# Kernel optimization log

Measured on AMD Instinct MI355X. Metric: run time of the kernel, lower is better.

The kernel has to match this reference:

```python
import jax, jax.numpy as jnp
import numpy as np

B, NQ, D, NH, DH = 16, 300, 256, 8, 32
L, P, FFN = 3, 4, 1024
LEVEL_SHAPES = [(80, 80), (40, 40), (20, 20)]
S = sum(h * w for h, w in LEVEL_SHAPES)  # 8400
EPS = 1e-5

PARAM_NAMES = ['wq', 'bq', 'wk', 'bk', 'wv', 'bv', 'wo', 'bo', 'ln1_g', 'ln1_b',
               'w_off', 'b_off', 'w_aw', 'b_aw', 'w_val', 'b_val', 'w_out', 'b_out',
               'ln2_g', 'ln2_b', 'w_fc1', 'b_fc1', 'w_fc2', 'b_fc2', 'ln3_g', 'ln3_b']


def _ln(x, g, b):
    m = jnp.mean(x, -1, keepdims=True)
    v = jnp.mean(jnp.square(x - m), -1, keepdims=True)
    return (x - m) * jax.lax.rsqrt(v + EPS) * g + b


def _bilinear(v_l, loc, Hl, Wl):
    # v_l: [B, Hl*Wl, NH, DH]; loc in [0,1]: [B, NQ, NH, P, 2]
    # matches torch grid_sample(align_corners=False, padding='zeros') with grid=2*loc-1
    x = loc[..., 0] * Wl - 0.5
    y = loc[..., 1] * Hl - 0.5
    x0 = jnp.floor(x)
    y0 = jnp.floor(y)
    vt = v_l.transpose(0, 2, 1, 3)  # [B, NH, Sl, DH]
    out = jnp.zeros((v_l.shape[0], NQ, NH, P, DH), v_l.dtype)
    for dx in (0, 1):
        for dy in (0, 1):
            xi = x0 + dx
            yi = y0 + dy
            w = (1.0 - jnp.abs(x - xi)) * (1.0 - jnp.abs(y - yi))
            valid = (xi >= 0) & (xi < Wl) & (yi >= 0) & (yi < Hl)
            idx = (jnp.clip(yi, 0, Hl - 1) * Wl + jnp.clip(xi, 0, Wl - 1)).astype(jnp.int32)
            idx_t = idx.transpose(0, 2, 1, 3).reshape(idx.shape[0], NH, NQ * P)
            g = jnp.take_along_axis(vt, idx_t[..., None], axis=2)  # [B, NH, NQ*P, DH]
            g = g.reshape(-1, NH, NQ, P, DH).transpose(0, 2, 1, 3, 4)
            out = out + g * (w * valid)[..., None]
    return out  # [B, NQ, NH, P, DH]


def _forward(hidden_states, pos_embed, encoder_hidden_states, reference_points, spatial_shapes, p):
    h = hidden_states
    # ---- self-attention (pos added to q and k only) ----
    hp = h + pos_embed
    q = (hp @ p['wq'] + p['bq']).reshape(B, NQ, NH, DH)
    k = (hp @ p['wk'] + p['bk']).reshape(B, NQ, NH, DH)
    v = (h @ p['wv'] + p['bv']).reshape(B, NQ, NH, DH)
    scores = jnp.einsum('bqhd,bkhd->bhqk', q, k) * (1.0 / np.sqrt(DH).astype(np.float32))
    attn = jax.nn.softmax(scores, -1)
    sa = jnp.einsum('bhqk,bkhd->bqhd', attn, v).reshape(B, NQ, D) @ p['wo'] + p['bo']
    h = _ln(h + sa, p['ln1_g'], p['ln1_b'])

    # ---- multiscale deformable cross-attention ----
    hp = h + pos_embed
    value = (encoder_hidden_states @ p['w_val'] + p['b_val']).reshape(B, S, NH, DH)
    off = (hp @ p['w_off'] + p['b_off']).reshape(B, NQ, NH, L, P, 2)
    aw = jax.nn.softmax((hp @ p['w_aw'] + p['b_aw']).reshape(B, NQ, NH, L * P), -1)
    aw = aw.reshape(B, NQ, NH, L, P)
    normalizer = jnp.stack([spatial_shapes[:, 1], spatial_shapes[:, 0]], -1).astype(h.dtype)  # [L,2] = (W,H)
    loc = reference_points[:, :, None, :, None, :] + off / normalizer[None, None, None, :, None, :]
    out = jnp.zeros((B, NQ, NH, DH), h.dtype)
    start = 0
    for l, (Hl, Wl) in enumerate(LEVEL_SHAPES):
        v_l = value[:, start:start + Hl * Wl]
        sampled = _bilinear(v_l, loc[:, :, :, l], Hl, Wl)  # [B,NQ,NH,P,DH]
        out = out + jnp.sum(sampled * aw[:, :, :, l, :, None], axis=3)
        start += Hl * Wl
    ca = out.reshape(B, NQ, D) @ p['w_out'] + p['b_out']
    h = _ln(h + ca, p['ln2_g'], p['ln2_b'])

    # ---- MLP ----
    mlp = jax.nn.relu(h @ p['w_fc1'] + p['b_fc1']) @ p['w_fc2'] + p['b_fc2']
    return _ln(h + mlp, p['ln3_g'], p['ln3_b'])


def setup_inputs() -> dict:
    key = jax.random.key(0)
    ks = iter(jax.random.split(key, 48))
    def nrm(shape, s=0.02):
        return jax.random.normal(next(ks), shape, jnp.float32) * s
    inp = {
        'hidden_states': jax.random.normal(next(ks), (B, NQ, D), jnp.float32),
        'pos_embed': jax.random.normal(next(ks), (B, NQ, D), jnp.float32),
        'encoder_hidden_states': jax.random.normal(next(ks), (B, S, D), jnp.float32),
        'reference_points': jax.random.uniform(next(ks), (B, NQ, L, 2), jnp.float32),
        'spatial_shapes': jnp.array(LEVEL_SHAPES, jnp.int32),
        'wq': nrm((D, D)), 'bq': jnp.zeros(D),
        'wk': nrm((D, D)), 'bk': jnp.zeros(D),
        'wv': nrm((D, D)), 'bv': jnp.zeros(D),
        'wo': nrm((D, D)), 'bo': jnp.zeros(D),
        'ln1_g': jnp.ones(D), 'ln1_b': jnp.zeros(D),
        'w_off': nrm((D, NH * L * P * 2)), 'b_off': nrm((NH * L * P * 2,), 0.1),
        'w_aw': nrm((D, NH * L * P)), 'b_aw': jnp.zeros(NH * L * P),
        'w_val': nrm((D, D)), 'b_val': jnp.zeros(D),
        'w_out': nrm((D, D)), 'b_out': jnp.zeros(D),
        'ln2_g': jnp.ones(D), 'ln2_b': jnp.zeros(D),
        'w_fc1': nrm((D, FFN)), 'b_fc1': jnp.zeros(FFN),
        'w_fc2': nrm((FFN, D)), 'b_fc2': jnp.zeros(D),
        'ln3_g': jnp.ones(D), 'ln3_b': jnp.zeros(D),
    }
    return inp


def reference(hidden_states, pos_embed, encoder_hidden_states, reference_points, spatial_shapes,
              wq, bq, wk, bk, wv, bv, wo, bo, ln1_g, ln1_b,
              w_off, b_off, w_aw, b_aw, w_val, b_val, w_out, b_out,
              ln2_g, ln2_b, w_fc1, b_fc1, w_fc2, b_fc2, ln3_g, ln3_b):
    p = dict(wq=wq, bq=bq, wk=wk, bk=bk, wv=wv, bv=bv, wo=wo, bo=bo,
             ln1_g=ln1_g, ln1_b=ln1_b, w_off=w_off, b_off=b_off, w_aw=w_aw, b_aw=b_aw,
             w_val=w_val, b_val=b_val, w_out=w_out, b_out=b_out, ln2_g=ln2_g, ln2_b=ln2_b,
             w_fc1=w_fc1, b_fc1=b_fc1, w_fc2=w_fc2, b_fc2=b_fc2, ln3_g=ln3_g, ln3_b=ln3_b)
    return _forward(hidden_states, pos_embed, encoder_hidden_states, reference_points, spatial_shapes, p)
```

## Files before the change

kernel.cpp:

```cpp
#include <hip/hip_runtime.h>
#include <hip/hip_bf16.h>
#include <math.h>

#define B_   16
#define NQ_  300
#define D_   256
#define NH_  8
#define DH_  32
#define L_   3
#define P_   4
#define FFN_ 1024
#define S_   8400
#define ROWS_ (B_*NQ_)
#define NB_   (ROWS_*D_)

typedef __attribute__((ext_vector_type(4))) unsigned short ushort4_t;
typedef __attribute__((ext_vector_type(8))) unsigned short ushort8_t;
typedef __attribute__((ext_vector_type(8))) short bf16x8;
typedef __attribute__((ext_vector_type(4))) float f32x4;

__device__ inline unsigned short f2b(float f) {
    __hip_bfloat16 h = __float2bfloat16(f);
    return __builtin_bit_cast(unsigned short, h);
}
__device__ inline float b2f(unsigned short u) {
    union { unsigned u; float f; } c; c.u = ((unsigned)u) << 16; return c.f;
}

__global__ __launch_bounds__(256) void prep_kernel(
    const float* __restrict__ wq, const float* __restrict__ wk,
    const float* __restrict__ wv, const float* __restrict__ wo,
    const float* __restrict__ w_val, const float* __restrict__ w_out,
    const float* __restrict__ w_off, const float* __restrict__ w_aw,
    const float* __restrict__ w_fc1, const float* __restrict__ w_fc2,
    const float* __restrict__ bq, const float* __restrict__ bk,
    const float* __restrict__ b_off, const float* __restrict__ b_aw,
    unsigned short* __restrict__ wtqk, unsigned short* __restrict__ wtv,
    unsigned short* __restrict__ wto, unsigned short* __restrict__ wtval,
    unsigned short* __restrict__ wtout, unsigned short* __restrict__ wtoa,
    unsigned short* __restrict__ wtfc1, unsigned short* __restrict__ wtfc2,
    float* __restrict__ bqk, float* __restrict__ boa)
{
    const int bid = blockIdx.x;
    if (bid >= 968) {
        int idx = (bid - 968)*256 + threadIdx.x;
        if (idx < 512) bqk[idx] = (idx < 256) ? bq[idx] : bk[idx-256];
        else { int j = idx - 512; if (j < 288) boa[j] = (j < 192) ? b_off[j] : b_aw[j-192]; }
        return;
    }
    const float* src; unsigned short* dst; int K, N, t;
    if      (bid < 64)  { src=wq;    dst=wtqk;         K=256;  N=256;  t=bid; }
    else if (bid < 128) { src=wk;    dst=wtqk+65536;   K=256;  N=256;  t=bid-64; }
    else if (bid < 192) { src=wv;    dst=wtv;          K=256;  N=256;  t=bid-128; }
    else if (bid < 256) { src=wo;    dst=wto;          K=256;  N=256;  t=bid-192; }
    else if (bid < 320) { src=w_val; dst=wtval;        K=256;  N=256;  t=bid-256; }
    else if (bid < 384) { src=w_out; dst=wtout;        K=256;  N=256;  t=bid-320; }
    else if (bid < 432) { src=w_off; dst=wtoa;         K=256;  N=192;  t=bid-384; }
    else if (bid < 456) { src=w_aw;  dst=wtoa+49152;   K=256;  N=96;   t=bid-432; }
    else if (bid < 712) { src=w_fc1; dst=wtfc1;        K=256;  N=1024; t=bid-456; }
    else                { src=w_fc2; dst=wtfc2;        K=1024; N=256;  t=bid-712; }

    __shared__ unsigned short tl[32][33];
    int tid = threadIdx.x;
    int tx = tid & 31, ty = tid >> 5;
    int ntx = N >> 5;
    int n0 = (t % ntx) * 32, k0 = (t / ntx) * 32;
    #pragma unroll
    for (int i = 0; i < 4; ++i)
        tl[tx][ty + i*8] = f2b(src[(size_t)(k0 + ty + i*8)*N + n0 + tx]);
    __syncthreads();
    #pragma unroll
    for (int i = 0; i < 4; ++i)
        dst[(size_t)(n0 + ty + i*8)*K + k0 + tx] = tl[ty + i*8][tx];
}

#define GEMM_PREAMBLE()                                                        \
    const int tid  = threadIdx.x;                                              \
    const int lane = tid & 63;                                                 \
    const int w    = tid >> 6;                                                 \
    const int wr   = w >> 1, wc = w & 1;                                       \
    const int m0   = blockIdx.y * 64;                                          \
    const int n0   = blockIdx.x * 128;                                         \
    const int fr   = lane & 15, fq = lane >> 4;                                \
    const int arow = tid >> 2, aseg = (tid & 3) * 8;                           \
    const int brow = tid >> 1, bseg = (tid & 1) * 16;                          \
    const bool a_ok = (m0 + arow) < M;                                         \
    const bool b_ok = (n0 + brow) < N;                                         \
    const float*          aptr  = A  + (size_t)(m0 + arow)*K + aseg;           \
    const float*          aptr2 = A2 ? A2 + (size_t)(m0 + arow)*K + aseg : (const float*)0; \
    const unsigned short* bptr  = WT + (size_t)(n0 + brow)*K + bseg;           \
    f32x4 acc[2][4];                                                           \
    _Pragma("unroll") for (int m = 0; m < 2; ++m)                              \
        _Pragma("unroll") for (int n = 0; n < 4; ++n)                          \
            acc[m][n] = (f32x4){0.f, 0.f, 0.f, 0.f};                           \
    float4 avA0, avB0, avA1, avB1;                                             \
    ushort8_t bvA0, bvB0, bvA1, bvB1;

#define GEMM_LOAD(avA, avB, bvA, bvB, kk) do {                                 \
    if (a_ok) {                                                                \
        avA = *(const float4*)(aptr + (kk));                                   \
        avB = *(const float4*)(aptr + (kk) + 4);                               \
        if (aptr2) {                                                           \
            float4 x2 = *(const float4*)(aptr2 + (kk));                        \
            float4 y2 = *(const float4*)(aptr2 + (kk) + 4);                    \
            avA.x += x2.x; avA.y += x2.y; avA.z += x2.z; avA.w += x2.w;        \
            avB.x += y2.x; avB.y += y2.y; avB.z += y2.z; avB.w += y2.w;        \
        }                                                                      \
    } else { avA = (float4){0,0,0,0}; avB = (float4){0,0,0,0}; }               \
    if (b_ok) { bvA = *(const ushort8_t*)(bptr + (kk));                        \
                bvB = *(const ushort8_t*)(bptr + (kk) + 8); }                  \
    else { _Pragma("unroll") for (int j = 0; j < 8; ++j){bvA[j]=0;bvB[j]=0;} } \
} while (0)

#define GEMM_STORE_LDS(avA, avB, bvA, bvB) do {                                \
    ushort8_t ac;                                                              \
    ac[0]=f2b(avA.x); ac[1]=f2b(avA.y); ac[2]=f2b(avA.z); ac[3]=f2b(avA.w);    \
    ac[4]=f2b(avB.x); ac[5]=f2b(avB.y); ac[6]=f2b(avB.z); ac[7]=f2b(avB.w);    \
    *(ushort8_t*)&As[arow][aseg]     = ac;                                     \
    *(ushort8_t*)&Bs[brow][bseg]     = bvA;                                    \
    *(ushort8_t*)&Bs[brow][bseg + 8] = bvB;                                    \
} while (0)

#define GEMM_COMPUTE() do {                                                    \
    bf16x8 af[2], bfv[4];                                                      \
    _Pragma("unroll") for (int m = 0; m < 2; ++m)                              \
        af[m] = *(const bf16x8*)&As[wr*32 + m*16 + fr][fq*8];                  \
    _Pragma("unroll") for (int n = 0; n < 4; ++n)                              \
        bfv[n] = *(const bf16x8*)&Bs[wc*64 + n*16 + fr][fq*8];                 \
    _Pragma("unroll") for (int m = 0; m < 2; ++m)                              \
        _Pragma("unroll") for (int n = 0; n < 4; ++n)                          \
            acc[m][n] = __builtin_amdgcn_mfma_f32_16x16x32_bf16(               \
                af[m], bfv[n], acc[m][n], 0, 0, 0);                            \
} while (0)

#define GEMM_KLOOP()                                                           \
    GEMM_LOAD(avA0, avB0, bvA0, bvB0, 0);                                      \
    for (int k0 = 0; k0 < K; k0 += 64) {                                       \
        __syncthreads();                                                       \
        GEMM_STORE_LDS(avA0, avB0, bvA0, bvB0);                                \
        GEMM_LOAD(avA1, avB1, bvA1, bvB1, k0 + 32);                            \
        __syncthreads();                                                       \
        GEMM_COMPUTE();                                                        \
        __syncthreads();                                                       \
        GEMM_STORE_LDS(avA1, avB1, bvA1, bvB1);                                \
        if (k0 + 64 < K) GEMM_LOAD(avA0, avB0, bvA0, bvB0, k0 + 64);           \
        __syncthreads();                                                       \
        GEMM_COMPUTE();                                                        \
    }

__global__ __launch_bounds__(256) void gemm_mfma64(
    const float* __restrict__ A, const float* __restrict__ A2,
    const unsigned short* __restrict__ WT,
    const float* __restrict__ bias, float* __restrict__ C,
    int M, int N, int K, int relu)
{
    __shared__ unsigned short As[64][40];
    __shared__ unsigned short Bs[128][40];
    GEMM_PREAMBLE();
    GEMM_KLOOP();

    #pragma unroll
    for (int n = 0; n < 4; ++n) {
        int col = n0 + wc*64 + n*16 + fr;
        if (col < N) {
            float bcol = bias[col];
            #pragma unroll
            for (int m = 0; m < 2; ++m) {
                int rbase = m0 + wr*32 + m*16 + fq*4;
                #pragma unroll
                for (int r = 0; r < 4; ++r) {
                    int row = rbase + r;
                    if (row < M) {
                        float vv = acc[m][n][r] + bcol;
                        if (relu) vv = fmaxf(vv, 0.f);
                        C[(size_t)row * N + col] = vv;
                    }
                }
            }
        }
    }
}

__global__ __launch_bounds__(256) void stage1_kernel(
    const float* __restrict__ ehs, const float* __restrict__ h_in,
    const float* __restrict__ pos,
    const unsigned short* __restrict__ wtval, const float* __restrict__ b_val,
    unsigned short* __restrict__ val_bf,
    const unsigned short* __restrict__ wtqk, const float* __restrict__ bqk,
    float* __restrict__ buf_qk,
    const unsigned short* __restrict__ wtv, const float* __restrict__ bv,
    float* __restrict__ buf_v)
{
    __shared__ unsigned short LDS[25600];

    const int bid  = blockIdx.x;
    const int tid  = threadIdx.x;
    const int lane = tid & 63;
    const int w    = tid >> 6;
    const int wr   = w >> 1, wc = w & 1;
    const int fr   = lane & 15, fq = lane >> 4;

    if (bid < 2100) {
        unsigned short (&As2)[2][64][40]  = *(unsigned short(*)[2][64][40])(LDS);
        unsigned short (&Bs2)[2][256][40] = *(unsigned short(*)[2][256][40])(LDS + 5120);
        const int m0 = bid * 64;

        f32x4 acc[2][8];
        #pragma unroll
        for (int m = 0; m < 2; ++m)
            #pragma unroll
            for (int n = 0; n < 8; ++n)
                acc[m][n] = (f32x4){0.f, 0.f, 0.f, 0.f};

        for (int kc = 0; kc < 4; ++kc) {
            const int kbase = kc * 64;
            __syncthreads();
            #pragma unroll
            for (int i = 0; i < 2; ++i) {
                int uf = i*256 + tid;
                int row = uf >> 3, j = uf & 7;
                const float* src = ehs + (size_t)(m0 + row)*256 + kbase + j*8;
                float4 x = *(const float4*)src;
                float4 y = *(const float4*)(src + 4);
                ushort8_t u;
                u[0]=f2b(x.x); u[1]=f2b(x.y); u[2]=f2b(x.z); u[3]=f2b(x.w);
                u[4]=f2b(y.x); u[5]=f2b(y.y); u[6]=f2b(y.z); u[7]=f2b(y.w);
                *(ushort8_t*)&As2[j>>2][row][(j&3)*8] = u;
            }
            #pragma unroll
            for (int i = 0; i < 8; ++i) {
                int uf = i*256 + tid;
                int row = uf >> 3, j = uf & 7;
                ushort8_t u = *(const ushort8_t*)(wtval + (size_t)row*256 + kbase + j*8);
                *(ushort8_t*)&Bs2[j>>2][row][(j&3)*8] = u;
            }
            __syncthreads();
            #pragma unroll
            for (int ks = 0; ks < 2; ++ks) {
                bf16x8 af[2], bfv[8];
                #pragma unroll
                for (int m = 0; m < 2; ++m)
                    af[m] = *(const bf16x8*)&As2[ks][wr*32 + m*16 + fr][fq*8];
                #pragma unroll
                for (int n = 0; n < 8; ++n)
                    bfv[n] = *(const bf16x8*)&Bs2[ks][wc*128 + n*16 + fr][fq*8];
                #pragma unroll
                for (int m = 0; m < 2; ++m)
                    #pragma unroll
                    for (int n = 0; n < 8; ++n)
                        acc[m][n] = __builtin_amdgcn_mfma_f32_16x16x32_bf16(
                            af[m], bfv[n], acc[m][n], 0, 0, 0);
            }
        }

        #pragma unroll
        for (int n = 0; n < 8; ++n) {
            int col = wc*128 + n*16 + fr;
            int hh = col >> 5, dd = col & 31;
            float bcol = b_val[col];
            #pragma unroll
            for (int m = 0; m < 2; ++m) {
                int rbase = m0 + wr*32 + m*16 + fq*4;
                #pragma unroll
                for (int r = 0; r < 4; ++r) {
                    unsigned row = rbase + r;
                    unsigned bb = row / (unsigned)S_;
                    unsigned ss = row - bb * (unsigned)S_;
                    val_bf[((size_t)(bb*NH_ + hh)*S_ + ss)*DH_ + dd] = f2b(acc[m][n][r] + bcol);
                }
            }
        }
    } else {
        unsigned short (&As)[64][40]  = *(unsigned short(*)[64][40])(LDS);
        unsigned short (&Bs)[128][40] = *(unsigned short(*)[128][40])(LDS + 2560);

        const int t = bid - 2100;
        int m0, n0, Ncols;
        const float* A2p = nullptr;
        const unsigned short* Bp; const float* bias; float* C;
        if (t < 300) {
            m0 = (t >> 2)*64; n0 = (t & 3)*128;
            A2p = pos; Bp = wtqk; bias = bqk; C = buf_qk; Ncols = 512;
        } else {
            int tt = t - 300;
            m0 = (tt >> 1)*64; n0 = (tt & 1)*128;
            Bp = wtv; bias = bv; C = buf_v; Ncols = 256;
        }

        const int arow = tid >> 2, aseg = (tid & 3) * 8;
        const int brow = tid >> 1, bseg = (tid & 1) * 16;
        const bool a_ok = true, b_ok = true;
        const int K = 256;
        const float*          aptr  = h_in + (size_t)(m0 + arow)*256 + aseg;
        const float*          aptr2 = A2p ? A2p + (size_t)(m0 + arow)*256 + aseg : (const float*)0;
        const unsigned short* bptr  = Bp + (size_t)(n0 + brow)*256 + bseg;

        f32x4 acc[2][4];
        #pragma unroll
        for (int m = 0; m < 2; ++m)
            #pragma unroll
            for (int n = 0; n < 4; ++n)
                acc[m][n] = (f32x4){0.f, 0.f, 0.f, 0.f};
        float4 avA0, avB0, avA1, avB1;
        ushort8_t bvA0, bvB0, bvA1, bvB1;

        GEMM_KLOOP();

        #pragma unroll
        for (int n = 0; n < 4; ++n) {
            int col = n0 + wc*64 + n*16 + fr;
            float bcol = bias[col];
            #pragma unroll
            for (int m = 0; m < 2; ++m) {
                int rbase = m0 + wr*32 + m*16 + fq*4;
                #pragma unroll
                for (int r = 0; r < 4; ++r)
                    C[(size_t)(rbase + r) * Ncols + col] = acc[m][n][r] + bcol;
            }
        }
    }
}

__global__ __launch_bounds__(256) void gemm_relu_bf16(
    const float* __restrict__ A, const unsigned short* __restrict__ WT,
    const float* __restrict__ bias, unsigned short* __restrict__ OUT,
    int M, int N, int K)
{
    __shared__ unsigned short As[64][40];
    __shared__ unsigned short Bs[128][40];
    const float* A2 = nullptr;
    GEMM_PREAMBLE();
    GEMM_KLOOP();

    #pragma unroll
    for (int n = 0; n < 4; ++n) {
        int col = n0 + wc*64 + n*16 + fr;
        float bcol = bias[col];
        #pragma unroll
        for (int m = 0; m < 2; ++m) {
            int rbase = m0 + wr*32 + m*16 + fq*4;
            #pragma unroll
            for (int r = 0; r < 4; ++r)
                OUT[(size_t)(rbase + r) * N + col] = f2b(fmaxf(acc[m][n][r] + bcol, 0.f));
        }
    }
}

#define GLN16_COMPUTE() do {                                                   \
    bf16x8 af = *(const bf16x8*)&As[fr][fq*8];                                 \
    _Pragma("unroll") for (int n = 0; n < 4; ++n) {                            \
        bf16x8 bfv = *(const bf16x8*)&Bs[w*64 + n*16 + fr][fq*8];              \
        acc[n] = __builtin_amdgcn_mfma_f32_16x16x32_bf16(af, bfv, acc[n], 0, 0, 0); \
    }                                                                          \
} while (0)

#define GLN16_EPILOGUE()                                                       \
    float gcol[4], bcol2[4], biascol[4];                                       \
    _Pragma("unroll") for (int n = 0; n < 4; ++n) {                            \
        int col = w*64 + n*16 + fr;                                            \
        biascol[n] = bias[col]; gcol[n] = g[col]; bcol2[n] = bb[col];          \
    }                                                                          \
    _Pragma("unroll") for (int r = 0; r < 4; ++r) {                            \
        int row = fq*4 + r;                                                    \
        float s = 0.f, sq = 0.f;                                               \
        _Pragma("unroll") for (int n = 0; n < 4; ++n) {                        \
            int col = w*64 + n*16 + fr;                                        \
            float vv = acc[n][r] + biascol[n]                                  \
                     + X[(size_t)(m0 + row)*256 + col];                        \
            acc[n][r] = vv; s += vv; sq += vv*vv;                              \
        }                                                                      \
        s  += __shfl_xor(s, 1);  sq += __shfl_xor(sq, 1);                      \
        s  += __shfl_xor(s, 2);  sq += __shfl_xor(sq, 2);                      \
        s  += __shfl_xor(s, 4);  sq += __shfl_xor(sq, 4);                      \
        s  += __shfl_xor(s, 8);  sq += __shfl_xor(sq, 8);                      \
        if (fr == 0) { psum[row][w] = s; psq[row][w] = sq; }                   \
    }                                                                          \
    __syncthreads();                                                           \
    _Pragma("unroll") for (int r = 0; r < 4; ++r) {                            \
        int row = fq*4 + r;                                                    \
        float mean = (psum[row][0]+psum[row][1]+psum[row][2]+psum[row][3]) * (1.0f/256.0f); \
        float ex2  = (psq[row][0]+psq[row][1]+psq[row][2]+psq[row][3]) * (1.0f/256.0f);     \
        float rstd = rsqrtf(ex2 - mean*mean + 1e-5f);                          \
        _Pragma("unroll") for (int n = 0; n < 4; ++n) {                        \
            int col = w*64 + n*16 + fr;                                        \
            OUT[(size_t)(m0 + row)*256 + col] =                                \
                (acc[n][r] - mean)*rstd*gcol[n] + bcol2[n];                    \
        }                                                                      \
    }

__global__ __launch_bounds__(256) void gemm_ln_f32A(
    const float* __restrict__ A, const unsigned short* __restrict__ WT,
    const float* __restrict__ bias, const float* __restrict__ X,
    const float* __restrict__ g, const float* __restrict__ bb,
    float* __restrict__ OUT, int K)
{
    __shared__ unsigned short As[16][40];
    __shared__ unsigned short Bs[256][40];
    __shared__ float psum[16][4], psq[16][4];

    const int tid  = threadIdx.x;
    const int lane = tid & 63;
    const int w    = tid >> 6;
    const int m0   = blockIdx.x * 16;
    const int fr   = lane & 15, fq = lane >> 4;
    const bool astage = tid < 64;
    const int arow = (tid >> 2) & 15, aseg = (tid & 3) * 8;
    const float*          aptr = A  + (size_t)(m0 + arow)*K + aseg;
    const unsigned short* bptr = WT + (size_t)tid*K;

    f32x4 acc[4];
    #pragma unroll
    for (int n = 0; n < 4; ++n) acc[n] = (f32x4){0.f, 0.f, 0.f, 0.f};

    float4 a0x = {0,0,0,0}, a0y = {0,0,0,0}, a1x = {0,0,0,0}, a1y = {0,0,0,0};
    ushort8_t b0[4], b1[4];

    if (astage) { a0x = *(const float4*)(aptr); a0y = *(const float4*)(aptr + 4); }
    #pragma unroll
    for (int j = 0; j < 4; ++j) b0[j] = *(const ushort8_t*)(bptr + j*8);
    for (int k0 = 0; k0 < K; k0 += 64) {
        __syncthreads();
        if (astage) {
            ushort8_t ac;
            ac[0]=f2b(a0x.x); ac[1]=f2b(a0x.y); ac[2]=f2b(a0x.z); ac[3]=f2b(a0x.w);
            ac[4]=f2b(a0y.x); ac[5]=f2b(a0y.y); ac[6]=f2b(a0y.z); ac[7]=f2b(a0y.w);
            *(ushort8_t*)&As[arow][aseg] = ac;
        }
        #pragma unroll
        for (int j = 0; j < 4; ++j) *(ushort8_t*)&Bs[tid][j*8] = b0[j];
        if (astage) { a1x = *(const float4*)(aptr + k0 + 32); a1y = *(const float4*)(aptr + k0 + 36); }
        #pragma unroll
        for (int j = 0; j < 4; ++j) b1[j] = *(const ushort8_t*)(bptr + k0 + 32 + j*8);
        __syncthreads();
        GLN16_COMPUTE();
        __syncthreads();
        if (astage) {
            ushort8_t ac;
            ac[0]=f2b(a1x.x); ac[1]=f2b(a1x.y); ac[2]=f2b(a1x.z); ac[3]=f2b(a1x.w);
            ac[4]=f2b(a1y.x); ac[5]=f2b(a1y.y); ac[6]=f2b(a1y.z); ac[7]=f2b(a1y.w);
            *(ushort8_t*)&As[arow][aseg] = ac;
        }
        #pragma unroll
        for (int j = 0; j < 4; ++j) *(ushort8_t*)&Bs[tid][j*8] = b1[j];
        if (k0 + 64 < K) {
            if (astage) { a0x = *(const float4*)(aptr + k0 + 64); a0y = *(const float4*)(aptr + k0 + 68); }
            #pragma unroll
            for (int j = 0; j < 4; ++j) b0[j] = *(const ushort8_t*)(bptr + k0 + 64 + j*8);
        }
        __syncthreads();
        GLN16_COMPUTE();
    }

    GLN16_EPILOGUE();
}

__global__ __launch_bounds__(256) void gemm_ln_bf16A(
    const unsigned short* __restrict__ A, const unsigned short* __restrict__ WT,
    const float* __restrict__ bias, const float* __restrict__ X,
    const float* __restrict__ g, const float* __restrict__ bb,
    float* __restrict__ OUT, int K)
{
    __shared__ unsigned short As[16][40];
    __shared__ unsigned short Bs[256][40];
    __shared__ float psum[16][4], psq[16][4];

    const int tid  = threadIdx.x;
    const int lane = tid & 63;
    const int w    = tid >> 6;
    const int m0   = blockIdx.x * 16;
    const int fr   = lane & 15, fq = lane >> 4;
    const bool astage = tid < 64;
    const int arow = (tid >> 2) & 15, aseg = (tid & 3) * 8;
    const unsigned short* aptr = A  + (size_t)(m0 + arow)*K + aseg;
    const unsigned short* bptr = WT + (size_t)tid*K;

    f32x4 acc[4];
    #pragma unroll
    for (int n = 0; n < 4; ++n) acc[n] = (f32x4){0.f, 0.f, 0.f, 0.f};

    ushort8_t a0, a1, b0[4], b1[4];
    #pragma unroll
    for (int j = 0; j < 8; ++j) { a0[j] = 0; a1[j] = 0; }

    if (astage) a0 = *(const ushort8_t*)(aptr);
    #pragma unroll
    for (int j = 0; j < 4; ++j) b0[j] = *(const ushort8_t*)(bptr + j*8);
    for (int k0 = 0; k0 < K; k0 += 64) {
        __syncthreads();
        if (astage) *(ushort8_t*)&As[arow][aseg] = a0;
        #pragma unroll
        for (int j = 0; j < 4; ++j) *(ushort8_t*)&Bs[tid][j*8] = b0[j];
        if (astage) a1 = *(const ushort8_t*)(aptr + k0 + 32);
        #pragma unroll
        for (int j = 0; j < 4; ++j) b1[j] = *(const ushort8_t*)(bptr + k0 + 32 + j*8);
        __syncthreads();
        GLN16_COMPUTE();
        __syncthreads();
        if (astage) *(ushort8_t*)&As[arow][aseg] = a1;
        #pragma unroll
        for (int j = 0; j < 4; ++j) *(ushort8_t*)&Bs[tid][j*8] = b1[j];
        if (k0 + 64 < K) {
            if (astage) a0 = *(const ushort8_t*)(aptr + k0 + 64);
            #pragma unroll
            for (int j = 0; j < 4; ++j) b0[j] = *(const ushort8_t*)(bptr + k0 + 64 + j*8);
        }
        __syncthreads();
        GLN16_COMPUTE();
    }

    GLN16_EPILOGUE();
}

__global__ __launch_bounds__(256) void self_attn_kernel(
    const float* __restrict__ qk, const float* __restrict__ v,
    float* __restrict__ sa)
{
    __shared__ unsigned short k_sw[304*32];
    __shared__ unsigned short vt[32][312];
    __shared__ unsigned short p_all[4][16][312];

    const int bid  = blockIdx.x;
    const int part = bid % 5;
    const int bh   = bid / 5;
    const int h    = bh & 7;
    const int b    = bh >> 3;
    const int tid  = threadIdx.x;
    const int lane = tid & 63;
    const int w    = tid >> 6;
    const int g    = lane >> 4;
    const int fr   = lane & 15;

    const size_t qbase = (size_t)b*NQ_*512 + h*DH_;
    const size_t kbase = qbase + 256;
    const size_t vbase = (size_t)b*NQ_*D_ + h*DH_;
    const size_t sbase = (size_t)b*NQ_*D_ + h*DH_;

    for (int i = tid; i < 1216; i += 256) {
        int r = i >> 2, u = i & 3;
        ushort8_t kb;
        if (r < NQ_) {
            const float* p8 = qk + kbase + (size_t)r*512 + u*8;
            float4 a0 = *(const float4*)p8;
            float4 a1 = *(const float4*)(p8 + 4);
            kb[0]=f2b(a0.x); kb[1]=f2b(a0.y); kb[2]=f2b(a0.z); kb[3]=f2b(a0.w);
            kb[4]=f2b(a1.x); kb[5]=f2b(a1.y); kb[6]=f2b(a1.z); kb[7]=f2b(a1.w);
        } else {
            #pragma unroll
            for (int j = 0; j < 8; ++j) kb[j] = 0;
        }
        int su = u ^ ((r >> 1) & 3);
        *(ushort8_t*)&k_sw[r*32 + su*8] = kb;
    }
    for (int i = tid; i < 1216; i += 256) {
        int kk = i >> 2, u = i & 3;
        if (kk < NQ_) {
            const float* p8 = v + vbase + (size_t)kk*D_ + u*8;
            float4 a0 = *(const float4*)p8;
            float4 a1 = *(const float4*)(p8 + 4);
            float f[8] = {a0.x,a0.y,a0.z,a0.w,a1.x,a1.y,a1.z,a1.w};
            #pragma unroll
            for (int j = 0; j < 8; ++j) vt[u*8 + j][kk] = f2b(f[j]);
        } else {
            #pragma unroll
            for (int j = 0; j < 8; ++j) vt[u*8 + j][kk] = 0;
        }
    }
    __syncthreads();

    const int q0 = part*64 + w*16;
    const int qi = q0 + fr;
    bf16x8 qf;
    if (qi < NQ_) {
        const float scale = 0.17677669529663687f;
        const float* p8 = qk + qbase + (size_t)qi*512 + g*8;
        float4 a0 = *(const float4*)p8;
        float4 a1 = *(const float4*)(p8 + 4);
        qf[0]=(short)f2b(a0.x*scale); qf[1]=(short)f2b(a0.y*scale);
        qf[2]=(short)f2b(a0.z*scale); qf[3]=(short)f2b(a0.w*scale);
        qf[4]=(short)f2b(a1.x*scale); qf[5]=(short)f2b(a1.y*scale);
        qf[6]=(short)f2b(a1.z*scale); qf[7]=(short)f2b(a1.w*scale);
    } else {
        #pragma unroll
        for (int j = 0; j < 8; ++j) qf[j] = 0;
    }

    const int ksw_u = g ^ ((fr >> 1) & 3);
    f32x4 acc[19];
    #pragma unroll
    for (int t = 0; t < 19; ++t) acc[t] = (f32x4){0.f,0.f,0.f,0.f};
    #pragma unroll
    for (int t = 0; t < 19; ++t) {
        int row = t*16 + fr;
        bf16x8 kf = *(const bf16x8*)&k_sw[row*32 + ksw_u*8];
        acc[t] = __builtin_amdgcn_mfma_f32_16x16x32_bf16(kf, qf, acc[t], 0, 0, 0);
    }
    if (g == 3) acc[18] = (f32x4){-1e30f, -1e30f, -1e30f, -1e30f};

    float m = -1e30f;
    #pragma unroll
    for (int t = 0; t < 19; ++t) {
        #pragma unroll
        for (int r = 0; r < 4; ++r) m = fmaxf(m, acc[t][r]);
    }
    m = fmaxf(m, __shfl_xor(m, 16));
    m = fmaxf(m, __shfl_xor(m, 32));
    float lsum = 0.f;
    #pragma unroll
    for (int t = 0; t < 19; ++t) {
        #pragma unroll
        for (int r = 0; r < 4; ++r) {
            float e = __expf(acc[t][r] - m);
            acc[t][r] = e;
            lsum += e;
        }
    }
    lsum += __shfl_xor(lsum, 16);
    lsum += __shfl_xor(lsum, 32);
    float inv = 1.0f / lsum;

    #pragma unroll
    for (int t = 0; t < 19; ++t) {
        ushort4_t pw = { f2b(acc[t][0]*inv), f2b(acc[t][1]*inv),
                         f2b(acc[t][2]*inv), f2b(acc[t][3]*inv) };
        *(ushort4_t*)&p_all[w][fr][t*16 + g*4] = pw;
    }

    f32x4 o0 = (f32x4){0.f,0.f,0.f,0.f};
    f32x4 o1 = (f32x4){0.f,0.f,0.f,0.f};
    #pragma unroll
    for (int ks = 0; ks < 10; ++ks) {
        int kb = ks*32 + g*8;
        bf16x8 pf, vf0, vf1;
        if (kb < 304) {
            pf  = *(const bf16x8*)&p_all[w][fr][kb];
            vf0 = *(const bf16x8*)&vt[fr][kb];
            vf1 = *(const bf16x8*)&vt[16 + fr][kb];
        } else {
            #pragma unroll
            for (int j = 0; j < 8; ++j) { pf[j] = 0; vf0[j] = 0; vf1[j] = 0; }
        }
        o0 = __builtin_amdgcn_mfma_f32_16x16x32_bf16(pf, vf0, o0, 0, 0, 0);
        o1 = __builtin_amdgcn_mfma_f32_16x16x32_bf16(pf, vf1, o1, 0, 0, 0);
    }

    #pragma unroll
    for (int r = 0; r < 4; ++r) {
        int qo = q0 + g*4 + r;
        if (qo < NQ_) {
            sa[sbase + (size_t)qo*D_ + fr]      = o0[r];
            sa[sbase + (size_t)qo*D_ + 16 + fr] = o1[r];
        }
    }
}

__global__ __launch_bounds__(256) void deform_kernel(
    const unsigned short* __restrict__ value, const float* __restrict__ oa,
    const float* __restrict__ refp, float* __restrict__ dout)
{
    int gid = blockIdx.x*256 + threadIdx.x;
    int l16 = gid & 15;
    int grp = gid >> 4;
    int h = grp & 7;
    int bq = grp >> 3;
    int qq = bq % NQ_;
    int b  = bq / NQ_;
    int d0 = l16*2;

    const int starts[3] = {0, 6400, 8000};
    const int Hs[3] = {80, 40, 20};

    const float* offp = oa + (size_t)(b*NQ_+qq)*288 + h*24;
    const float* awp  = oa + (size_t)(b*NQ_+qq)*288 + 192 + h*12;
    const float* refq = refp + (size_t)(b*NQ_+qq)*(L_*2);
    const unsigned short* vb = value + ((size_t)(b*NH_ + h)*S_)*DH_ + d0;

    float av[12];
    float mx = -1e30f;
    #pragma unroll
    for (int i = 0; i < 12; ++i) { av[i] = awp[i]; mx = fmaxf(mx, av[i]); }
    float ssum = 0.f;
    #pragma unroll
    for (int i = 0; i < 12; ++i) { av[i] = __expf(av[i]-mx); ssum += av[i]; }
    float sinv = 1.f / ssum;

    float acc0 = 0.f, acc1 = 0.f;
    #pragma unroll
    for (int l = 0; l < L_; l++) {
        int Hl = Hs[l], Wl = Hs[l];
        float rx = refq[l*2+0], ry = refq[l*2+1];
        const unsigned short* vlb = vb + (size_t)starts[l]*DH_;
        #pragma unroll
        for (int p = 0; p < P_; p++) {
            float ox = offp[(l*P_+p)*2+0], oy = offp[(l*P_+p)*2+1];
            float a  = av[l*P_+p] * sinv;
            float x = (rx + ox/(float)Wl)*(float)Wl - 0.5f;
            float y = (ry + oy/(float)Hl)*(float)Hl - 0.5f;
            float x0 = floorf(x), y0 = floorf(y);
            #pragma unroll
            for (int dy = 0; dy < 2; dy++) {
                #pragma unroll
                for (int dx = 0; dx < 2; dx++) {
                    float xi = x0 + dx, yi = y0 + dy;
                    float wgt = (1.f - fabsf(x-xi))*(1.f - fabsf(y-yi));
                    bool valid = (xi >= 0.f) && (xi < (float)Wl) && (yi >= 0.f) && (yi < (float)Hl);
                    if (valid && wgt != 0.f) {
                        int ix = (int)xi, iy = (int)yi;
                        unsigned u = *(const unsigned*)(vlb + (size_t)(iy*Wl + ix)*DH_);
                        float aw2 = a * wgt;
                        acc0 += aw2 * b2f((unsigned short)(u & 0xffff));
                        acc1 += aw2 * b2f((unsigned short)(u >> 16));
                    }
                }
            }
        }
    }
    float2 o = { acc0, acc1 };
    *(float2*)&dout[(size_t)grp*32 + d0] = o;
}

extern "C" void kernel_launch(void* const* d_in, const int* in_sizes, int n_in,
                              void* d_out, int out_size, void* d_ws, size_t ws_size,
                              hipStream_t stream) {
    (void)in_sizes; (void)n_in; (void)out_size; (void)ws_size;
    const float* h_in  = (const float*)d_in[0];
    const float* pos   = (const float*)d_in[1];
    const float* ehs   = (const float*)d_in[2];
    const float* refp  = (const float*)d_in[3];
    const float* wq    = (const float*)d_in[5];
    const float* bq    = (const float*)d_in[6];
    const float* wk    = (const float*)d_in[7];
    const float* bk    = (const float*)d_in[8];
    const float* wv    = (const float*)d_in[9];
    const float* bv    = (const float*)d_in[10];
    const float* wo    = (const float*)d_in[11];
    const float* bo    = (const float*)d_in[12];
    const float* ln1g  = (const float*)d_in[13];
    const float* ln1b  = (const float*)d_in[14];
    const float* w_off = (const float*)d_in[15];
    const float* b_off = (const float*)d_in[16];
    const float* w_aw  = (const float*)d_in[17];
    const float* b_aw  = (const float*)d_in[18];
    const float* w_val = (const float*)d_in[19];
    const float* b_val = (const float*)d_in[20];
    const float* w_out = (const float*)d_in[21];
    const float* b_out = (const float*)d_in[22];
    const float* ln2g  = (const float*)d_in[23];
    const float* ln2b  = (const float*)d_in[24];
    const float* w_fc1 = (const float*)d_in[25];
    const float* b_fc1 = (const float*)d_in[26];
    const float* w_fc2 = (const float*)d_in[27];
    const float* b_fc2 = (const float*)d_in[28];
    const float* ln3g  = (const float*)d_in[29];
    const float* ln3b  = (const float*)d_in[30];
    float* out = (float*)d_out;

    float* ws = (float*)d_ws;
    float* buf_qk   = ws + 1*(size_t)NB_;
    float* buf_v    = ws + 3*(size_t)NB_;
    float* buf_sa   = ws + 4*(size_t)NB_;
    float* buf_h1   = ws + 6*(size_t)NB_;
    float* buf_h2   = ws + 7*(size_t)NB_;
    float* buf_oa   = ws + 8*(size_t)NB_;
    unsigned short* fc1_bf = (unsigned short*)(ws + 9*(size_t)NB_ + NB_/2);
    unsigned short* val_bf = (unsigned short*)(ws + 13*(size_t)NB_ + NB_/2);

    unsigned short* wtb = (unsigned short*)(ws + 27*(size_t)NB_ + NB_/2);
    unsigned short* wtqk  = wtb;
    unsigned short* wtv   = wtqk  + 131072;
    unsigned short* wto   = wtv   + 65536;
    unsigned short* wtval = wto   + 65536;
    unsigned short* wtout = wtval + 65536;
    unsigned short* wtoa  = wtout + 65536;
    unsigned short* wtfc1 = wtoa  + 73728;
    unsigned short* wtfc2 = wtfc1 + 262144;
    float* bqk = (float*)(wtfc2 + 262144);
    float* boa = bqk + 512;

    dim3 blk(256);

    prep_kernel<<<dim3(972), blk, 0, stream>>>(
        wq, wk, wv, wo, w_val, w_out, w_off, w_aw, w_fc1, w_fc2,
        bq, bk, b_off, b_aw,
        wtqk, wtv, wto, wtval, wtout, wtoa, wtfc1, wtfc2, bqk, boa);

    stage1_kernel<<<dim3(2550), blk, 0, stream>>>(
        ehs, h_in, pos, wtval, b_val, val_bf, wtqk, bqk, buf_qk, wtv, bv, buf_v);

    self_attn_kernel<<<dim3(B_*NH_*5), blk, 0, stream>>>(buf_qk, buf_v, buf_sa);
    gemm_ln_f32A<<<dim3(ROWS_/16), blk, 0, stream>>>(
        buf_sa, wto, bo, h_in, ln1g, ln1b, buf_h1, 256);
    gemm_mfma64<<<dim3(3, 75), blk, 0, stream>>>(buf_h1, pos, wtoa, boa, buf_oa, ROWS_, 288, D_, 0);
    deform_kernel<<<dim3(ROWS_*NH_*16/256), blk, 0, stream>>>(val_bf, buf_oa, refp, buf_v);
    gemm_ln_f32A<<<dim3(ROWS_/16), blk, 0, stream>>>(
        buf_v, wtout, b_out, buf_h1, ln2g, ln2b, buf_h2, 256);
    gemm_relu_bf16<<<dim3(8, 75), blk, 0, stream>>>(buf_h2, wtfc1, b_fc1, fc1_bf, ROWS_, FFN_, D_);
    gemm_ln_bf16A<<<dim3(ROWS_/16), blk, 0, stream>>>(
        fc1_bf, wtfc2, b_fc2, buf_h2, ln3g, ln3b, out, FFN_);
}
```

Measured before the change: 211.3 us.

## Store q/k/v and self-attention output in bf16, widen deform gather

The stage1 q/k and v projections now write bf16 instead of fp32. The self-attention kernel reads these bf16 buffers directly and writes a bf16 output, which the output-projection LN GEMM consumes through its bf16-A variant. Separately, the deformable sampling kernel now has each thread handle 4 channels with 64-bit loads instead of 2 channels with 32-bit loads, halving the thread count. This is meant to cut global memory traffic on the intermediates, and it adds one more bf16 rounding of q before scaling.

```diff
diff --git a/kernel.cpp b/kernel.cpp
--- a/kernel.cpp
+++ b/kernel.cpp
@@ -187,9 +187,9 @@
     const unsigned short* __restrict__ wtval, const float* __restrict__ b_val,
     unsigned short* __restrict__ val_bf,
     const unsigned short* __restrict__ wtqk, const float* __restrict__ bqk,
-    float* __restrict__ buf_qk,
+    unsigned short* __restrict__ qk_bf,
     const unsigned short* __restrict__ wtv, const float* __restrict__ bv,
-    float* __restrict__ buf_v)
+    unsigned short* __restrict__ v_bf)
 {
     __shared__ unsigned short LDS[25600];
 
@@ -277,14 +277,14 @@
         const int t = bid - 2100;
         int m0, n0, Ncols;
         const float* A2p = nullptr;
-        const unsigned short* Bp; const float* bias; float* C;
+        const unsigned short* Bp; const float* bias; unsigned short* C;
         if (t < 300) {
             m0 = (t >> 2)*64; n0 = (t & 3)*128;
-            A2p = pos; Bp = wtqk; bias = bqk; C = buf_qk; Ncols = 512;
+            A2p = pos; Bp = wtqk; bias = bqk; C = qk_bf; Ncols = 512;
         } else {
             int tt = t - 300;
             m0 = (tt >> 1)*64; n0 = (tt & 1)*128;
-            Bp = wtv; bias = bv; C = buf_v; Ncols = 256;
+            Bp = wtv; bias = bv; C = v_bf; Ncols = 256;
         }
 
         const int arow = tid >> 2, aseg = (tid & 3) * 8;
@@ -315,7 +315,7 @@
                 int rbase = m0 + wr*32 + m*16 + fq*4;
                 #pragma unroll
                 for (int r = 0; r < 4; ++r)
-                    C[(size_t)(rbase + r) * Ncols + col] = acc[m][n][r] + bcol;
+                    C[(size_t)(rbase + r) * Ncols + col] = f2b(acc[m][n][r] + bcol);
             }
         }
     }
@@ -512,8 +512,8 @@
 }
 
 __global__ __launch_bounds__(256) void self_attn_kernel(
-    const float* __restrict__ qk, const float* __restrict__ v,
-    float* __restrict__ sa)
+    const unsigned short* __restrict__ qk, const unsigned short* __restrict__ v,
+    unsigned short* __restrict__ sa)
 {
     __shared__ unsigned short k_sw[304*32];
     __shared__ unsigned short vt[32][312];
@@ -539,11 +539,7 @@
         int r = i >> 2, u = i & 3;
         ushort8_t kb;
         if (r < NQ_) {
-            const float* p8 = qk + kbase + (size_t)r*512 + u*8;
-            float4 a0 = *(const float4*)p8;
-            float4 a1 = *(const float4*)(p8 + 4);
-            kb[0]=f2b(a0.x); kb[1]=f2b(a0.y); kb[2]=f2b(a0.z); kb[3]=f2b(a0.w);
-            kb[4]=f2b(a1.x); kb[5]=f2b(a1.y); kb[6]=f2b(a1.z); kb[7]=f2b(a1.w);
+            kb = *(const ushort8_t*)(qk + kbase + (size_t)r*512 + u*8);
         } else {
             #pragma unroll
             for (int j = 0; j < 8; ++j) kb[j] = 0;
@@ -554,12 +550,9 @@
     for (int i = tid; i < 1216; i += 256) {
         int kk = i >> 2, u = i & 3;
         if (kk < NQ_) {
-            const float* p8 = v + vbase + (size_t)kk*D_ + u*8;
-            float4 a0 = *(const float4*)p8;
-            float4 a1 = *(const float4*)(p8 + 4);
-            float f[8] = {a0.x,a0.y,a0.z,a0.w,a1.x,a1.y,a1.z,a1.w};
-            #pragma unroll
-            for (int j = 0; j < 8; ++j) vt[u*8 + j][kk] = f2b(f[j]);
+            ushort8_t vv = *(const ushort8_t*)(v + vbase + (size_t)kk*D_ + u*8);
+            #pragma unroll
+            for (int j = 0; j < 8; ++j) vt[u*8 + j][kk] = vv[j];
         } else {
             #pragma unroll
             for (int j = 0; j < 8; ++j) vt[u*8 + j][kk] = 0;
@@ -572,13 +565,9 @@
     bf16x8 qf;
     if (qi < NQ_) {
         const float scale = 0.17677669529663687f;
-        const float* p8 = qk + qbase + (size_t)qi*512 + g*8;
-        float4 a0 = *(const float4*)p8;
-        float4 a1 = *(const float4*)(p8 + 4);
-        qf[0]=(short)f2b(a0.x*scale); qf[1]=(short)f2b(a0.y*scale);
-        qf[2]=(short)f2b(a0.z*scale); qf[3]=(short)f2b(a0.w*scale);
-        qf[4]=(short)f2b(a1.x*scale); qf[5]=(short)f2b(a1.y*scale);
-        qf[6]=(short)f2b(a1.z*scale); qf[7]=(short)f2b(a1.w*scale);
+        ushort8_t q8 = *(const ushort8_t*)(qk + qbase + (size_t)qi*512 + g*8);
+        #pragma unroll
+        for (int j = 0; j < 8; ++j) qf[j] = (short)f2b(b2f(q8[j]) * scale);
     } else {
         #pragma unroll
         for (int j = 0; j < 8; ++j) qf[j] = 0;
@@ -647,8 +636,8 @@
     for (int r = 0; r < 4; ++r) {
         int qo = q0 + g*4 + r;
         if (qo < NQ_) {
-            sa[sbase + (size_t)qo*D_ + fr]      = o0[r];
-            sa[sbase + (size_t)qo*D_ + 16 + fr] = o1[r];
+            sa[sbase + (size_t)qo*D_ + fr]      = f2b(o0[r]);
+            sa[sbase + (size_t)qo*D_ + 16 + fr] = f2b(o1[r]);
         }
     }
 }
@@ -658,13 +647,13 @@
     const float* __restrict__ refp, float* __restrict__ dout)
 {
     int gid = blockIdx.x*256 + threadIdx.x;
-    int l16 = gid & 15;
-    int grp = gid >> 4;
+    int l8 = gid & 7;
+    int grp = gid >> 3;
     int h = grp & 7;
     int bq = grp >> 3;
     int qq = bq % NQ_;
     int b  = bq / NQ_;
-    int d0 = l16*2;
+    int d0 = l8*4;
 
     const int starts[3] = {0, 6400, 8000};
     const int Hs[3] = {80, 40, 20};
@@ -683,7 +672,7 @@
     for (int i = 0; i < 12; ++i) { av[i] = __expf(av[i]-mx); ssum += av[i]; }
     float sinv = 1.f / ssum;
 
-    float acc0 = 0.f, acc1 = 0.f;
+    float acc0 = 0.f, acc1 = 0.f, acc2 = 0.f, acc3 = 0.f;
     #pragma unroll
     for (int l = 0; l < L_; l++) {
         int Hl = Hs[l], Wl = Hs[l];
@@ -705,17 +694,19 @@
                     bool valid = (xi >= 0.f) && (xi < (float)Wl) && (yi >= 0.f) && (yi < (float)Hl);
                     if (valid && wgt != 0.f) {
                         int ix = (int)xi, iy = (int)yi;
-                        unsigned u = *(const unsigned*)(vlb + (size_t)(iy*Wl + ix)*DH_);
+                        uint2 u2 = *(const uint2*)(vlb + (size_t)(iy*Wl + ix)*DH_);
                         float aw2 = a * wgt;
-                        acc0 += aw2 * b2f((unsigned short)(u & 0xffff));
-                        acc1 += aw2 * b2f((unsigned short)(u >> 16));
+                        acc0 += aw2 * b2f((unsigned short)(u2.x & 0xffff));
+                        acc1 += aw2 * b2f((unsigned short)(u2.x >> 16));
+                        acc2 += aw2 * b2f((unsigned short)(u2.y & 0xffff));
+                        acc3 += aw2 * b2f((unsigned short)(u2.y >> 16));
                     }
                 }
             }
         }
     }
-    float2 o = { acc0, acc1 };
-    *(float2*)&dout[(size_t)grp*32 + d0] = o;
+    float4 o = { acc0, acc1, acc2, acc3 };
+    *(float4*)&dout[(size_t)grp*32 + d0] = o;
 }
 
 extern "C" void kernel_launch(void* const* d_in, const int* in_sizes, int n_in,
@@ -755,9 +746,10 @@
     float* out = (float*)d_out;
 
     float* ws = (float*)d_ws;
-    float* buf_qk   = ws + 1*(size_t)NB_;
-    float* buf_v    = ws + 3*(size_t)NB_;
-    float* buf_sa   = ws + 4*(size_t)NB_;
+    unsigned short* qk_bf = (unsigned short*)(ws + 1*(size_t)NB_);
+    unsigned short* v_bf  = qk_bf + (size_t)ROWS_*512;
+    unsigned short* sa_bf = v_bf + (size_t)ROWS_*256;
+    float* buf_dout = ws + 3*(size_t)NB_;
     float* buf_h1   = ws + 6*(size_t)NB_;
     float* buf_h2   = ws + 7*(size_t)NB_;
     float* buf_oa   = ws + 8*(size_t)NB_;
@@ -784,15 +776,15 @@
         wtqk, wtv, wto, wtval, wtout, wtoa, wtfc1, wtfc2, bqk, boa);
 
     stage1_kernel<<<dim3(2550), blk, 0, stream>>>(
-        ehs, h_in, pos, wtval, b_val, val_bf, wtqk, bqk, buf_qk, wtv, bv, buf_v);
-
-    self_attn_kernel<<<dim3(B_*NH_*5), blk, 0, stream>>>(buf_qk, buf_v, buf_sa);
+        ehs, h_in, pos, wtval, b_val, val_bf, wtqk, bqk, qk_bf, wtv, bv, v_bf);
+
+    self_attn_kernel<<<dim3(B_*NH_*5), blk, 0, stream>>>(qk_bf, v_bf, sa_bf);
+    gemm_ln_bf16A<<<dim3(ROWS_/16), blk, 0, stream>>>(
+        sa_bf, wto, bo, h_in, ln1g, ln1b, buf_h1, 256);
+    gemm_mfma64<<<dim3(3, 75), blk, 0, stream>>>(buf_h1, pos, wtoa, boa, buf_oa, ROWS_, 288, D_, 0);
+    deform_kernel<<<dim3(ROWS_*NH_*8/256), blk, 0, stream>>>(val_bf, buf_oa, refp, buf_dout);
     gemm_ln_f32A<<<dim3(ROWS_/16), blk, 0, stream>>>(
-        buf_sa, wto, bo, h_in, ln1g, ln1b, buf_h1, 256);
-    gemm_mfma64<<<dim3(3, 75), blk, 0, stream>>>(buf_h1, pos, wtoa, boa, buf_oa, ROWS_, 288, D_, 0);
-    deform_kernel<<<dim3(ROWS_*NH_*16/256), blk, 0, stream>>>(val_bf, buf_oa, refp, buf_v);
-    gemm_ln_f32A<<<dim3(ROWS_/16), blk, 0, stream>>>(
-        buf_v, wtout, b_out, buf_h1, ln2g, ln2b, buf_h2, 256);
+        buf_dout, wtout, b_out, buf_h1, ln2g, ln2b, buf_h2, 256);
     gemm_relu_bf16<<<dim3(8, 75), blk, 0, stream>>>(buf_h2, wtfc1, b_fc1, fc1_bf, ROWS_, FFN_, D_);
     gemm_ln_bf16A<<<dim3(ROWS_/16), blk, 0, stream>>>(
         fc1_bf, wtfc2, b_fc2, buf_h2, ln3g, ln3b, out, FFN_);
```

Result: faster. 192.8 us (-8.8%).
